# Kernel optimization log

Hardware: AMD Instinct MI355X
Metric: run time of the kernel (lower is better)

Reference implementation:

```python
import jax, jax.numpy as jnp
import numpy as np

N = 80000      # nodes
E = 1280000    # edges
G = 64         # graphs in batch
CIN = 128
D = 64
NUM_LAYERS = 6


def setup_inputs() -> dict:
    key = jax.random.key(0)
    ks = jax.random.split(key, 12)
    s = 0.05
    return {
        "x": jax.random.normal(ks[0], (N, CIN), jnp.float32),
        "edge_index": jax.random.randint(ks[1], (2, E), 0, N, dtype=jnp.int32),
        "batch": jnp.sort(jax.random.randint(ks[2], (N,), 0, G, dtype=jnp.int32)),
        "W_in": jax.random.normal(ks[3], (CIN, D), jnp.float32) * s,
        "b_in": jnp.zeros((D,), jnp.float32),
        "W_hid": jax.random.normal(ks[4], (NUM_LAYERS - 1, D, D), jnp.float32) * s,
        "b_hid": jnp.zeros((NUM_LAYERS - 1, D), jnp.float32),
        "lin1_w": jax.random.normal(ks[5], (2 * D, 64), jnp.float32) * s,
        "lin1_b": jnp.zeros((64,), jnp.float32),
        "lin2_w": jax.random.normal(ks[6], (64, 64), jnp.float32) * s,
        "lin2_b": jnp.zeros((64,), jnp.float32),
        "lin3_w": jax.random.normal(ks[7], (64, 1), jnp.float32) * s,
        "lin3_b": jnp.zeros((1,), jnp.float32),
    }


def _gcn_norm(edge_index, n):
    # PyG gcn_norm: add self-loops, symmetric D^-1/2 (A+I) D^-1/2 normalization
    loops = jnp.arange(n, dtype=edge_index.dtype)
    src = jnp.concatenate([edge_index[0], loops])
    dst = jnp.concatenate([edge_index[1], loops])
    deg = jax.ops.segment_sum(jnp.ones_like(src, jnp.float32), dst, num_segments=n)
    dinv = jnp.where(deg > 0, jax.lax.rsqrt(jnp.maximum(deg, 1.0)), 0.0)
    norm = dinv[src] * dinv[dst]
    return src, dst, norm


def _gcn_conv(x, W, b, src, dst, norm, n):
    h = x @ W                                   # [N, D]
    msg = h[src] * norm[:, None]                # [E+N, D] gather + scale
    out = jax.ops.segment_sum(msg, dst, num_segments=n)
    return out + b


def reference(x, edge_index, batch, W_in, b_in, W_hid, b_hid,
              lin1_w, lin1_b, lin2_w, lin2_b, lin3_w, lin3_b):
    n = x.shape[0]
    src, dst, norm = _gcn_norm(edge_index, n)
    # layer 0: in_channels -> D, then ReLU
    h = jax.nn.relu(_gcn_conv(x, W_in, b_in, src, dst, norm, n))
    # hidden layers: ReLU on all but the last conv
    n_hid = W_hid.shape[0]
    for i in range(n_hid):
        h = _gcn_conv(h, W_hid[i], b_hid[i], src, dst, norm, n)
        if i != n_hid - 1:
            h = jax.nn.relu(h)
    # global add + max pooling per graph
    x1 = jax.ops.segment_sum(h, batch, num_segments=G)   # [G, D]
    x2 = jax.ops.segment_max(h, batch, num_segments=G)   # [G, D]
    g = jnp.concatenate([x1, x2], axis=1)                # [G, 2D]
    g = jax.nn.relu(g @ lin1_w + lin1_b)
    g = jax.nn.relu(g @ lin2_w + lin2_b)
    return g @ lin3_w + lin3_b                           # [G, 1]
```

## Files before the change

### kernel.cpp

```cpp
#include <hip/hip_runtime.h>
#include <hip/hip_bf16.h>
#include <cstdint>
#include <cstddef>


#define FEAT 64

static __device__ inline unsigned short f2bf(float f) {
  unsigned u = __float_as_uint(f);
  unsigned r = (u + 0x7FFF + ((u >> 16) & 1)) >> 16;
  return (unsigned short)r;
}
static __device__ inline float bf2f(unsigned short u) {
  return __uint_as_float(((unsigned)u) << 16);
}


__global__ __launch_bounds__(256) void init_kernel(int* deg, int* cursor,
    float* gsum, unsigned int* gmax, int n) {
  int i = blockIdx.x * 256 + threadIdx.x;
  if (i < n) { deg[i] = 0; cursor[i] = 0; }
  if (i < 64 * FEAT) { gsum[i] = 0.f; gmax[i] = 0xFF800000u; }
}

__global__ __launch_bounds__(256) void hist_kernel(const int* __restrict__ dst,
    int* __restrict__ deg, int e, int n) {
  const int slice = blockIdx.x & 7;
  const int lo = slice * (n >> 3);
  const int hi = lo + (n >> 3);
  const int nb = gridDim.x >> 3;
  const int bid = blockIdx.x >> 3;
  for (int i = bid * 256 + threadIdx.x; i < e; i += nb * 256) {
    int d = dst[i];
    if (d >= lo && d < hi) atomicAdd(&deg[d], 1);
  }
}

__global__ __launch_bounds__(256) void dinv_kernel(const int* __restrict__ deg,
    float* __restrict__ dinv, int n) {
  int i = blockIdx.x * 256 + threadIdx.x;
  if (i < n) dinv[i] = rsqrtf((float)(deg[i] + 1));
}

__global__ __launch_bounds__(256) void scan1_kernel(const int* __restrict__ deg,
    int* __restrict__ offs, int* __restrict__ bsums, int n) {
  __shared__ int buf[256];
  int t = threadIdx.x;
  int i = blockIdx.x * 256 + t;
  int v = (i < n) ? deg[i] : 0;
  buf[t] = v;
  __syncthreads();
  for (int off = 1; off < 256; off <<= 1) {
    int add = (t >= off) ? buf[t - off] : 0;
    __syncthreads();
    buf[t] += add;
    __syncthreads();
  }
  if (i < n) offs[i] = buf[t] - v;
  if (t == 255) bsums[blockIdx.x] = buf[255];
}

__global__ __launch_bounds__(512) void scan2_kernel(int* bs, int nb) {
  __shared__ int buf[512];
  int t = threadIdx.x;
  int v = (t < nb) ? bs[t] : 0;
  buf[t] = v;
  __syncthreads();
  for (int off = 1; off < 512; off <<= 1) {
    int add = (t >= off) ? buf[t - off] : 0;
    __syncthreads();
    buf[t] += add;
    __syncthreads();
  }
  if (t < nb) bs[t] = buf[t] - v;
}

__global__ __launch_bounds__(256) void scan3_kernel(int* __restrict__ offs,
    const int* __restrict__ bs, int n) {
  int i = blockIdx.x * 256 + threadIdx.x;
  if (i < n) offs[i] += bs[blockIdx.x];
}

__global__ __launch_bounds__(256) void fill_kernel(const int* __restrict__ src,
    const int* __restrict__ dst, const int* __restrict__ offs,
    int* __restrict__ cursor, int* __restrict__ csr_src, int e, int n) {
  const int slice = blockIdx.x & 7;
  const int lo = slice * (n >> 3);
  const int hi = lo + (n >> 3);
  const int nb = gridDim.x >> 3;
  const int bid = blockIdx.x >> 3;
  for (int i = bid * 256 + threadIdx.x; i < e; i += nb * 256) {
    int d = dst[i];
    if (d >= lo && d < hi) {
      int pos = offs[d] + atomicAdd(&cursor[d], 1);
      csr_src[pos] = src[i];
    }
  }
}

template <int K>
__global__ __launch_bounds__(256, 2) void gemm_kernel(
    const float* __restrict__ in, const float* __restrict__ W,
    const float* __restrict__ dinv, unsigned short* __restrict__ tg, int n) {
  __shared__ float in_lds[64 * K];
  const int lane = threadIdx.x & 63;
  const int wid = threadIdx.x >> 6;

  float wreg[K];
#pragma unroll
  for (int k = 0; k < K; ++k) wreg[k] = W[k * 64 + lane];

  const int ntiles = n >> 6;
  for (int tile = blockIdx.x; tile < ntiles; tile += gridDim.x) {
    const float* tin = in + (size_t)tile * 64 * K;
    __syncthreads();
#pragma unroll
    for (int i = threadIdx.x; i < 16 * K; i += 256)
      *(float4*)&in_lds[i * 4] = *(const float4*)&tin[i * 4];
    __syncthreads();

    unsigned short* tout = tg + (size_t)tile * 64 * 64;
    const float* dvp = dinv + tile * 64;
#pragma unroll
    for (int g = 0; g < 4; ++g) {
      const int r0 = wid * 16 + g * 4;
      float a0 = 0.f, a1 = 0.f, a2 = 0.f, a3 = 0.f;
#pragma unroll
      for (int k = 0; k < K; k += 4) {
        float4 x0 = *(const float4*)&in_lds[(r0 + 0) * K + k];
        float4 x1 = *(const float4*)&in_lds[(r0 + 1) * K + k];
        float4 x2 = *(const float4*)&in_lds[(r0 + 2) * K + k];
        float4 x3 = *(const float4*)&in_lds[(r0 + 3) * K + k];
        a0 = fmaf(x0.x, wreg[k + 0], a0); a0 = fmaf(x0.y, wreg[k + 1], a0);
        a0 = fmaf(x0.z, wreg[k + 2], a0); a0 = fmaf(x0.w, wreg[k + 3], a0);
        a1 = fmaf(x1.x, wreg[k + 0], a1); a1 = fmaf(x1.y, wreg[k + 1], a1);
        a1 = fmaf(x1.z, wreg[k + 2], a1); a1 = fmaf(x1.w, wreg[k + 3], a1);
        a2 = fmaf(x2.x, wreg[k + 0], a2); a2 = fmaf(x2.y, wreg[k + 1], a2);
        a2 = fmaf(x2.z, wreg[k + 2], a2); a2 = fmaf(x2.w, wreg[k + 3], a2);
        a3 = fmaf(x3.x, wreg[k + 0], a3); a3 = fmaf(x3.y, wreg[k + 1], a3);
        a3 = fmaf(x3.z, wreg[k + 2], a3); a3 = fmaf(x3.w, wreg[k + 3], a3);
      }
      tout[(r0 + 0) * 64 + lane] = f2bf(a0 * dvp[r0 + 0]);
      tout[(r0 + 1) * 64 + lane] = f2bf(a1 * dvp[r0 + 1]);
      tout[(r0 + 2) * 64 + lane] = f2bf(a2 * dvp[r0 + 2]);
      tout[(r0 + 3) * 64 + lane] = f2bf(a3 * dvp[r0 + 3]);
    }
  }
}

__global__ __launch_bounds__(256) void agg_kernel(
    const unsigned short* __restrict__ tg, const int* __restrict__ csr_src,
    const int* __restrict__ offs, const int* __restrict__ cnt,
    const float* __restrict__ dinv, const float* __restrict__ bias,
    float* __restrict__ h, int n, int relu) {
  int wave = (blockIdx.x * 256 + threadIdx.x) >> 6;
  int lane = threadIdx.x & 63;
  if (wave >= n) return;
  int v = wave;
  float acc = bf2f(tg[(size_t)v * 64 + lane]);
  int j = offs[v];
  int end = j + cnt[v];
  for (; j + 3 < end; j += 4) {
    int s0 = csr_src[j + 0], s1 = csr_src[j + 1];
    int s2 = csr_src[j + 2], s3 = csr_src[j + 3];
    unsigned short u0 = tg[(size_t)s0 * 64 + lane];
    unsigned short u1 = tg[(size_t)s1 * 64 + lane];
    unsigned short u2 = tg[(size_t)s2 * 64 + lane];
    unsigned short u3 = tg[(size_t)s3 * 64 + lane];
    acc += bf2f(u0) + bf2f(u1) + bf2f(u2) + bf2f(u3);
  }
  for (; j < end; ++j) {
    int s = csr_src[j];
    acc += bf2f(tg[(size_t)s * 64 + lane]);
  }
  acc = fmaf(dinv[v], acc, bias[lane]);
  if (relu) acc = fmaxf(acc, 0.f);
  h[(size_t)v * 64 + lane] = acc;
}


__device__ inline void atomic_max_float(float* addr, float val) {
  if (val >= 0.f)
    atomicMax((int*)addr, __float_as_int(val));
  else
    atomicMin((unsigned int*)addr, (unsigned int)__float_as_int(val));
}

#define POOL_CHUNK 128

__global__ __launch_bounds__(256) void pool_kernel(const float* __restrict__ h,
    const int* __restrict__ batch, float* __restrict__ gsum,
    float* __restrict__ gmax, int n) {
  int wave = (blockIdx.x * 256 + threadIdx.x) >> 6;
  int lane = threadIdx.x & 63;
  int start = wave * POOL_CHUNK;
  if (start >= n) return;
  int end = min(start + POOL_CHUNK, n);
  float s = 0.f, m = -INFINITY;
  int cur = batch[start];
  for (int v = start; v < end; ++v) {
    int g = batch[v];
    if (g != cur) {
      atomicAdd(&gsum[cur * 64 + lane], s);
      atomic_max_float(&gmax[cur * 64 + lane], m);
      s = 0.f; m = -INFINITY; cur = g;
    }
    float x = h[(size_t)v * 64 + lane];
    s += x;
    m = fmaxf(m, x);
  }
  atomicAdd(&gsum[cur * 64 + lane], s);
  atomic_max_float(&gmax[cur * 64 + lane], m);
}


__global__ __launch_bounds__(256) void mlp_kernel(const float* __restrict__ gsum,
    const float* __restrict__ gmax, const float* __restrict__ w1,
    const float* __restrict__ b1, const float* __restrict__ w2,
    const float* __restrict__ b2, const float* __restrict__ w3,
    const float* __restrict__ b3, float* __restrict__ out) {
  __shared__ float smem[64 * 128 + 64 * 64];
  float* gg = smem;
  float* z1 = smem + 64 * 128;
  int t = threadIdx.x;
  for (int i = t; i < 64 * 128; i += 256) {
    int g = i >> 7, f = i & 127;
    gg[i] = (f < 64) ? gsum[g * 64 + f] : gmax[g * 64 + (f - 64)];
  }
  __syncthreads();
  for (int i = t; i < 64 * 64; i += 256) {
    int g = i >> 6, j = i & 63;
    float acc = b1[j];
    for (int f = 0; f < 128; ++f) acc = fmaf(gg[(g << 7) + f], w1[f * 64 + j], acc);
    z1[i] = fmaxf(acc, 0.f);
  }
  __syncthreads();
  float* z2 = smem;
  for (int i = t; i < 64 * 64; i += 256) {
    int g = i >> 6, j = i & 63;
    float acc = b2[j];
    for (int f = 0; f < 64; ++f) acc = fmaf(z1[(g << 6) + f], w2[f * 64 + j], acc);
    z2[i] = fmaxf(acc, 0.f);
  }
  __syncthreads();
  if (t < 64) {
    float acc = b3[0];
    for (int j = 0; j < 64; ++j) acc = fmaf(z2[(t << 6) + j], w3[j], acc);
    out[t] = acc;
  }
}


extern "C" void kernel_launch(void* const* d_in, const int* in_sizes, int n_in,
                              void* d_out, int out_size, void* d_ws, size_t ws_size,
                              hipStream_t stream) {
  const float* x      = (const float*)d_in[0];
  const int*   eidx   = (const int*)d_in[1];
  const int*   batch  = (const int*)d_in[2];
  const float* W_in   = (const float*)d_in[3];
  const float* b_in   = (const float*)d_in[4];
  const float* W_hid  = (const float*)d_in[5];
  const float* b_hid  = (const float*)d_in[6];
  const float* lin1_w = (const float*)d_in[7];
  const float* lin1_b = (const float*)d_in[8];
  const float* lin2_w = (const float*)d_in[9];
  const float* lin2_b = (const float*)d_in[10];
  const float* lin3_w = (const float*)d_in[11];
  const float* lin3_b = (const float*)d_in[12];
  float* out = (float*)d_out;

  const int N = in_sizes[2];
  const int E = in_sizes[1] / 2;
  const int CIN = in_sizes[0] / N;
  const int n_hid = in_sizes[5] / (64 * 64);

  const int* src = eidx;
  const int* dst = eidx + E;

  char* ws = (char*)d_ws;
  size_t off = 0;
  auto alloc = [&](size_t bytes) {
    size_t o = off;
    off = (off + bytes + 255) & ~(size_t)255;
    return o;
  };
  int*            deg     = (int*)(ws + alloc((size_t)N * 4));
  int*            cursor  = (int*)(ws + alloc((size_t)N * 4));
  float*          dinv    = (float*)(ws + alloc((size_t)N * 4));
  int*            offs    = (int*)(ws + alloc((size_t)N * 4));
  int*            bsums   = (int*)(ws + alloc(1024 * 4));
  int*            csr_src = (int*)(ws + alloc((size_t)E * 4));
  unsigned short* tg      = (unsigned short*)(ws + alloc((size_t)N * 64 * 2));
  float*          hbuf    = (float*)(ws + alloc((size_t)N * 64 * 4));
  float*          gsum    = (float*)(ws + alloc(64 * 64 * 4));
  float*          gmax    = (float*)(ws + alloc(64 * 64 * 4));
  (void)ws_size; (void)n_in; (void)out_size; (void)CIN;

  const int nbN = (N + 255) / 256;

  init_kernel<<<nbN, 256, 0, stream>>>(deg, cursor, gsum, (unsigned int*)gmax, N);
  hist_kernel<<<1024, 256, 0, stream>>>(dst, deg, E, N);
  dinv_kernel<<<nbN, 256, 0, stream>>>(deg, dinv, N);
  scan1_kernel<<<nbN, 256, 0, stream>>>(deg, offs, bsums, N);
  scan2_kernel<<<1, 512, 0, stream>>>(bsums, nbN);
  scan3_kernel<<<nbN, 256, 0, stream>>>(offs, bsums, N);
  fill_kernel<<<1024, 256, 0, stream>>>(src, dst, offs, cursor, csr_src, E, N);

  const int ntiles = N >> 6;
  const int agg_blocks = (N * 64 + 255) / 256;

  gemm_kernel<128><<<ntiles, 256, 0, stream>>>(x, W_in, dinv, tg, N);
  agg_kernel<<<agg_blocks, 256, 0, stream>>>(tg, csr_src, offs, deg,
                                             dinv, b_in, hbuf, N, 1);
  for (int i = 0; i < n_hid; ++i) {
    gemm_kernel<64><<<ntiles, 256, 0, stream>>>(hbuf, W_hid + (size_t)i * 64 * 64,
                                                dinv, tg, N);
    agg_kernel<<<agg_blocks, 256, 0, stream>>>(tg, csr_src, offs, deg,
                                               dinv, b_hid + (size_t)i * 64, hbuf, N,
                                               (i != n_hid - 1) ? 1 : 0);
  }

  const int pool_waves = (N + POOL_CHUNK - 1) / POOL_CHUNK;
  const int pool_blocks = (pool_waves * 64 + 255) / 256;
  pool_kernel<<<pool_blocks, 256, 0, stream>>>(hbuf, batch, gsum, gmax, N);

  mlp_kernel<<<1, 256, 0, stream>>>(gsum, gmax, lin1_w, lin1_b, lin2_w, lin2_b,
                                    lin3_w, lin3_b, out);
}
```

Measured before the change: 730.8 us.

## Fuse next-layer GEMM into aggregation kernel with ping-pong bf16 buffers

```diff
diff --git a/kernel.cpp b/kernel.cpp
--- a/kernel.cpp
+++ b/kernel.cpp
@@ -148,34 +148,87 @@
   }
 }
 
-__global__ __launch_bounds__(256) void agg_kernel(
-    const unsigned short* __restrict__ tg, const int* __restrict__ csr_src,
+__global__ __launch_bounds__(256) void agg_mid_kernel(
+    const unsigned short* __restrict__ tg_in, const int* __restrict__ csr_src,
     const int* __restrict__ offs, const int* __restrict__ cnt,
     const float* __restrict__ dinv, const float* __restrict__ bias,
-    float* __restrict__ h, int n, int relu) {
-  int wave = (blockIdx.x * 256 + threadIdx.x) >> 6;
-  int lane = threadIdx.x & 63;
-  if (wave >= n) return;
-  int v = wave;
-  float acc = bf2f(tg[(size_t)v * 64 + lane]);
+    const float* __restrict__ Wn, unsigned short* __restrict__ tg_out, int n) {
+  __shared__ float hrow[4][64];
+  const int lane = threadIdx.x & 63;
+  const int wid = threadIdx.x >> 6;
+
+  float wn[64];
+#pragma unroll
+  for (int f = 0; f < 64; ++f) wn[f] = Wn[f * 64 + lane];
+
+  int v = (blockIdx.x * 256 + threadIdx.x) >> 6;
+  if (v >= n) return;
+
+  float acc = bf2f(tg_in[(size_t)v * 64 + lane]);
   int j = offs[v];
   int end = j + cnt[v];
-  for (; j + 3 < end; j += 4) {
+  for (; j + 7 < end; j += 8) {
     int s0 = csr_src[j + 0], s1 = csr_src[j + 1];
     int s2 = csr_src[j + 2], s3 = csr_src[j + 3];
-    unsigned short u0 = tg[(size_t)s0 * 64 + lane];
-    unsigned short u1 = tg[(size_t)s1 * 64 + lane];
-    unsigned short u2 = tg[(size_t)s2 * 64 + lane];
-    unsigned short u3 = tg[(size_t)s3 * 64 + lane];
-    acc += bf2f(u0) + bf2f(u1) + bf2f(u2) + bf2f(u3);
-  }
-  for (; j < end; ++j) {
-    int s = csr_src[j];
-    acc += bf2f(tg[(size_t)s * 64 + lane]);
-  }
-  acc = fmaf(dinv[v], acc, bias[lane]);
-  if (relu) acc = fmaxf(acc, 0.f);
-  h[(size_t)v * 64 + lane] = acc;
+    int s4 = csr_src[j + 4], s5 = csr_src[j + 5];
+    int s6 = csr_src[j + 6], s7 = csr_src[j + 7];
+    float t0 = bf2f(tg_in[(size_t)s0 * 64 + lane]);
+    float t1 = bf2f(tg_in[(size_t)s1 * 64 + lane]);
+    float t2 = bf2f(tg_in[(size_t)s2 * 64 + lane]);
+    float t3 = bf2f(tg_in[(size_t)s3 * 64 + lane]);
+    float t4 = bf2f(tg_in[(size_t)s4 * 64 + lane]);
+    float t5 = bf2f(tg_in[(size_t)s5 * 64 + lane]);
+    float t6 = bf2f(tg_in[(size_t)s6 * 64 + lane]);
+    float t7 = bf2f(tg_in[(size_t)s7 * 64 + lane]);
+    acc += ((t0 + t1) + (t2 + t3)) + ((t4 + t5) + (t6 + t7));
+  }
+  for (; j < end; ++j)
+    acc += bf2f(tg_in[(size_t)csr_src[j] * 64 + lane]);
+
+  float h = fmaxf(fmaf(dinv[v], acc, bias[lane]), 0.f);
+
+  hrow[wid][lane] = h;
+  float tval = 0.f;
+#pragma unroll
+  for (int f = 0; f < 64; f += 4) {
+    float4 h4 = *(const float4*)&hrow[wid][f];
+    tval = fmaf(h4.x, wn[f + 0], tval);
+    tval = fmaf(h4.y, wn[f + 1], tval);
+    tval = fmaf(h4.z, wn[f + 2], tval);
+    tval = fmaf(h4.w, wn[f + 3], tval);
+  }
+  tg_out[(size_t)v * 64 + lane] = f2bf(dinv[v] * tval);
+}
+
+__global__ __launch_bounds__(256) void agg_last_kernel(
+    const unsigned short* __restrict__ tg_in, const int* __restrict__ csr_src,
+    const int* __restrict__ offs, const int* __restrict__ cnt,
+    const float* __restrict__ dinv, const float* __restrict__ bias,
+    float* __restrict__ h, int n) {
+  int v = (blockIdx.x * 256 + threadIdx.x) >> 6;
+  int lane = threadIdx.x & 63;
+  if (v >= n) return;
+  float acc = bf2f(tg_in[(size_t)v * 64 + lane]);
+  int j = offs[v];
+  int end = j + cnt[v];
+  for (; j + 7 < end; j += 8) {
+    int s0 = csr_src[j + 0], s1 = csr_src[j + 1];
+    int s2 = csr_src[j + 2], s3 = csr_src[j + 3];
+    int s4 = csr_src[j + 4], s5 = csr_src[j + 5];
+    int s6 = csr_src[j + 6], s7 = csr_src[j + 7];
+    float t0 = bf2f(tg_in[(size_t)s0 * 64 + lane]);
+    float t1 = bf2f(tg_in[(size_t)s1 * 64 + lane]);
+    float t2 = bf2f(tg_in[(size_t)s2 * 64 + lane]);
+    float t3 = bf2f(tg_in[(size_t)s3 * 64 + lane]);
+    float t4 = bf2f(tg_in[(size_t)s4 * 64 + lane]);
+    float t5 = bf2f(tg_in[(size_t)s5 * 64 + lane]);
+    float t6 = bf2f(tg_in[(size_t)s6 * 64 + lane]);
+    float t7 = bf2f(tg_in[(size_t)s7 * 64 + lane]);
+    acc += ((t0 + t1) + (t2 + t3)) + ((t4 + t5) + (t6 + t7));
+  }
+  for (; j < end; ++j)
+    acc += bf2f(tg_in[(size_t)csr_src[j] * 64 + lane]);
+  h[(size_t)v * 64 + lane] = fmaf(dinv[v], acc, bias[lane]);
 }
 
 
@@ -290,7 +343,8 @@
   int*            offs    = (int*)(ws + alloc((size_t)N * 4));
   int*            bsums   = (int*)(ws + alloc(1024 * 4));
   int*            csr_src = (int*)(ws + alloc((size_t)E * 4));
-  unsigned short* tg      = (unsigned short*)(ws + alloc((size_t)N * 64 * 2));
+  unsigned short* tg_a    = (unsigned short*)(ws + alloc((size_t)N * 64 * 2));
+  unsigned short* tg_b    = (unsigned short*)(ws + alloc((size_t)N * 64 * 2));
   float*          hbuf    = (float*)(ws + alloc((size_t)N * 64 * 4));
   float*          gsum    = (float*)(ws + alloc(64 * 64 * 4));
   float*          gmax    = (float*)(ws + alloc(64 * 64 * 4));
@@ -309,16 +363,19 @@
   const int ntiles = N >> 6;
   const int agg_blocks = (N * 64 + 255) / 256;
 
-  gemm_kernel<128><<<ntiles, 256, 0, stream>>>(x, W_in, dinv, tg, N);
-  agg_kernel<<<agg_blocks, 256, 0, stream>>>(tg, csr_src, offs, deg,
-                                             dinv, b_in, hbuf, N, 1);
-  for (int i = 0; i < n_hid; ++i) {
-    gemm_kernel<64><<<ntiles, 256, 0, stream>>>(hbuf, W_hid + (size_t)i * 64 * 64,
-                                                dinv, tg, N);
-    agg_kernel<<<agg_blocks, 256, 0, stream>>>(tg, csr_src, offs, deg,
-                                               dinv, b_hid + (size_t)i * 64, hbuf, N,
-                                               (i != n_hid - 1) ? 1 : 0);
-  }
+  gemm_kernel<128><<<ntiles, 256, 0, stream>>>(x, W_in, dinv, tg_a, N);
+
+  unsigned short* cur = tg_a;
+  unsigned short* nxt = tg_b;
+  for (int k = 0; k < n_hid; ++k) {
+    const float* bias_k = (k == 0) ? b_in : (b_hid + (size_t)(k - 1) * 64);
+    agg_mid_kernel<<<agg_blocks, 256, 0, stream>>>(
+        cur, csr_src, offs, deg, dinv, bias_k,
+        W_hid + (size_t)k * 64 * 64, nxt, N);
+    unsigned short* t = cur; cur = nxt; nxt = t;
+  }
+  agg_last_kernel<<<agg_blocks, 256, 0, stream>>>(
+      cur, csr_src, offs, deg, dinv, b_hid + (size_t)(n_hid - 1) * 64, hbuf, N);
 
   const int pool_waves = (N + POOL_CHUNK - 1) / POOL_CHUNK;
   const int pool_blocks = (pool_waves * 64 + 255) / 256;
```

New measurement: 970.8 us. 1.33x slower.
